# Kernel optimization log

Hardware: AMD Instinct MI355X
Metric: run time of the kernel (lower is better)

Reference implementation:

```python
import math
import jax, jax.numpy as jnp
import numpy as np

DILATIONS = (1, 2, 3)

def conv2d(x, w, b, d=1, p=0):
    # x: NCHW, w: OIHW
    y = jax.lax.conv_general_dilated(
        x, w, window_strides=(1, 1), padding=[(p, p), (p, p)],
        rhs_dilation=(d, d), dimension_numbers=('NCHW', 'OIHW', 'NCHW'))
    return y + b[None, :, None, None]

def setup_inputs() -> dict:
    key = jax.random.key(0)
    ks = jax.random.split(key, 6)
    B, C, H = 2, 256, 96
    inner = 256 // 18  # = 14
    f = lambda k, s, sc: jax.random.normal(k, s, dtype=jnp.float32) * sc
    return {
        'x':        f(ks[0], (B, C, H, H), 1.0),
        'proj_w':   f(ks[1], (C, C, 1, 1), 0.06),
        'proj_b':   jnp.zeros((C,), jnp.float32),
        'reduce_w': f(ks[2], (inner, C, 1, 1), 0.06),
        'reduce_b': jnp.zeros((inner,), jnp.float32),
        'dil_w':    f(ks[3], (3, inner, inner, 3, 3), 0.08),
        'dil_b':    jnp.zeros((3, inner), jnp.float32),
        'fuse_w':   f(ks[4], (C, inner * 3 * 6, 1, 1), 0.06),
        'fuse_b':   jnp.zeros((C,), jnp.float32),
    }

def reference(x, proj_w, proj_b, reduce_w, reduce_b, dil_w, dil_b, fuse_w, fuse_b):
    B, C, H, W = x.shape
    # PatchEmbed (1x1 conv, stride 1) then PatchUnEmbed is identity on layout
    fmap = conv2d(x, proj_w, proj_b)                    # (B,C,H,W)
    # SAMSNLMFilter
    xr = conv2d(fmap, reduce_w, reduce_b)               # (B,inner,H,W)
    tfs = [xr,
           jnp.flip(xr, -1),
           jnp.flip(xr, -2),
           jnp.rot90(xr, 1, (-2, -1)),
           jnp.rot90(xr, 2, (-2, -1)),
           jnp.rot90(xr, 3, (-2, -1))]
    feats = []
    for i, d in enumerate(DILATIONS):
        co = conv2d(xr, dil_w[i], dil_b[i], d=d, p=d)   # (B,inner,H,W)
        feats.extend(co * t for t in tfs)
    fused = conv2d(jnp.concatenate(feats, axis=1), fuse_w, fuse_b)  # (B,C,H,W)
    tok = fused.reshape(B, C, H * W).transpose(0, 2, 1)             # (B,N,C)
    scale = 1.0 / math.sqrt(C)
    scores = jnp.einsum('bnc,bmc->bnm', tok, tok) * scale           # (B,N,N)
    attn = jax.nn.softmax(scores, axis=-1)
    out = jnp.einsum('bnm,bmc->bnc', attn, tok)
    out = out.transpose(0, 2, 1).reshape(B, C, H, W)
    return fmap + 0.2 * out  # residual_scale default 0.2
```

## Files before the change

kernel.cpp:

```cpp
#include <hip/hip_runtime.h>
#include <hip/hip_bf16.h>

#define NB 2
#define CH 256
#define HS 96
#define HW 9216
#define CHW 2359296
#define INNER 14
#define NF 252
#define SL2E 0.09016844f

using f32x4 = __attribute__((ext_vector_type(4))) float;
using s16x8 = __attribute__((ext_vector_type(8))) short;

template<int CIN, typename OT>
__global__ __launch_bounds__(256)
void k_conv1x1(const float* __restrict__ in, const float* __restrict__ w,
               const float* __restrict__ bias, OT* __restrict__ out) {
    __shared__ float wsh[CIN][32];
    const int tid = threadIdx.x;
    const int coB = blockIdx.y * 32;
    for (int e = tid; e < CIN * 32; e += 256) {
        int ci = e >> 5, col = e & 31;
        wsh[ci][col] = w[(coB + col) * CIN + ci];
    }
    __syncthreads();
    const int P0  = blockIdx.x * 512 + tid;
    const int b   = P0 / HW;
    const int pp0 = P0 - b * HW;
    const int pp1 = pp0 + 256;
    const float* inb = in + (size_t)b * CIN * HW;
    float acc0[32], acc1[32];
    #pragma unroll
    for (int j = 0; j < 32; ++j) { acc0[j] = 0.f; acc1[j] = 0.f; }
    for (int ci = 0; ci < CIN; ++ci) {
        float x0 = inb[(size_t)ci * HW + pp0];
        float x1 = inb[(size_t)ci * HW + pp1];
        const float4* wr = (const float4*)wsh[ci];
        #pragma unroll
        for (int q = 0; q < 8; ++q) {
            float4 wv = wr[q];
            acc0[q*4+0] += wv.x*x0; acc0[q*4+1] += wv.y*x0;
            acc0[q*4+2] += wv.z*x0; acc0[q*4+3] += wv.w*x0;
            acc1[q*4+0] += wv.x*x1; acc1[q*4+1] += wv.y*x1;
            acc1[q*4+2] += wv.z*x1; acc1[q*4+3] += wv.w*x1;
        }
    }
    OT* ob = out + (size_t)b * CH * HW;
    #pragma unroll
    for (int j = 0; j < 32; ++j) {
        float bv = bias[coB + j];
        ob[(size_t)(coB + j) * HW + pp0] = (OT)(acc0[j] + bv);
        ob[(size_t)(coB + j) * HW + pp1] = (OT)(acc1[j] + bv);
    }
}

__global__ __launch_bounds__(256)
void k_reduce(const float* __restrict__ fmap, const float* __restrict__ w,
              const float* __restrict__ bias, float* __restrict__ xr) {
    __shared__ float wsh[256][16];
    __shared__ float part[4][64][17];
    const int tid = threadIdx.x;
    for (int e = tid; e < 256 * 16; e += 256) {
        int ci = e >> 4, co = e & 15;
        wsh[ci][co] = (co < INNER) ? w[co * 256 + ci] : 0.f;
    }
    __syncthreads();
    const int px  = tid & 63, grp = tid >> 6;
    const int Pb  = blockIdx.x * 64;
    const int b   = Pb / HW;
    const int ppb = Pb - b * HW;
    const float* fb = fmap + (size_t)b * CHW + (size_t)(grp * 64) * HW + ppb + px;
    float acc[16];
    #pragma unroll
    for (int j = 0; j < 16; ++j) acc[j] = 0.f;
    for (int ci = 0; ci < 64; ++ci) {
        float xv = fb[(size_t)ci * HW];
        const float4* wr = (const float4*)wsh[grp * 64 + ci];
        #pragma unroll
        for (int q = 0; q < 4; ++q) {
            float4 wv = wr[q];
            acc[q*4+0] += wv.x*xv; acc[q*4+1] += wv.y*xv;
            acc[q*4+2] += wv.z*xv; acc[q*4+3] += wv.w*xv;
        }
    }
    #pragma unroll
    for (int j = 0; j < 16; ++j) part[grp][px][j] = acc[j];
    __syncthreads();
    for (int e = tid; e < 64 * INNER; e += 256) {
        int co = e >> 6, p2 = e & 63;
        float v = part[0][p2][co] + part[1][p2][co] + part[2][p2][co] +
                  part[3][p2][co] + bias[co];
        xr[(size_t)(b * INNER + co) * HW + ppb + p2] = v;
    }
}

__global__ __launch_bounds__(256)
void k_dil(const float* __restrict__ xr, const float* __restrict__ dw,
           const float* __restrict__ db, float* __restrict__ feats) {
    int bid = blockIdx.x;
    const int hb = bid % 36; bid /= 36;
    const int oc = bid % 14; bid /= 14;
    const int b  = bid & 1;  bid >>= 1;
    const int d  = bid;
    const int dil = d + 1;
    __shared__ float wsh[126];
    const int tid = threadIdx.x;
    if (tid < 126) wsh[tid] = dw[(d * 14 + oc) * 126 + tid];
    __syncthreads();
    const int p = hb * 256 + tid;
    const int h = p / 96, w = p - (p / 96) * 96;
    const float* xb = xr + (size_t)b * INNER * HW;
    float acc = db[d * 14 + oc];
    for (int ic = 0; ic < 14; ++ic) {
        const float* xc = xb + (size_t)ic * HW;
        #pragma unroll
        for (int kh = 0; kh < 3; ++kh) {
            int ih = h + (kh - 1) * dil;
            if (ih < 0 || ih >= 96) continue;
            #pragma unroll
            for (int kw = 0; kw < 3; ++kw) {
                int iw = w + (kw - 1) * dil;
                if (iw < 0 || iw >= 96) continue;
                acc += xc[ih * 96 + iw] * wsh[ic * 9 + kh * 3 + kw];
            }
        }
    }
    const float* xo = xb + (size_t)oc * HW;
    const int H1 = 95;
    float t0 = xo[h * 96 + w];
    float t1 = xo[h * 96 + (H1 - w)];
    float t2 = xo[(H1 - h) * 96 + w];
    float t3 = xo[w * 96 + (H1 - h)];
    float t4 = xo[(H1 - h) * 96 + (H1 - w)];
    float t5 = xo[(H1 - w) * 96 + h];
    float* fo = feats + (size_t)b * NF * HW;
    const int ch0 = d * 6 * 14 + oc;
    fo[(size_t)(ch0 + 0 * 14) * HW + p] = acc * t0;
    fo[(size_t)(ch0 + 1 * 14) * HW + p] = acc * t1;
    fo[(size_t)(ch0 + 2 * 14) * HW + p] = acc * t2;
    fo[(size_t)(ch0 + 3 * 14) * HW + p] = acc * t3;
    fo[(size_t)(ch0 + 4 * 14) * HW + p] = acc * t4;
    fo[(size_t)(ch0 + 5 * 14) * HW + p] = acc * t5;
}

__global__ __launch_bounds__(256)
void k_tr(const unsigned short* __restrict__ tc, unsigned short* __restrict__ tt) {
    const int tid = threadIdx.x;
    int bid = blockIdx.x;
    const int b = bid / 576;
    const int r = bid - b * 576;
    const int t0 = (r >> 2) * 64;
    const int c0 = (r & 3) * 64;
    __shared__ unsigned int T[64][37];
    const unsigned short* tcb = tc + (size_t)b * CHW;
    unsigned short* ttb = tt + (size_t)b * CHW;
    for (int e = tid; e < 2048; e += 256) {
        int to = e & 63, chp = e >> 6;
        unsigned int v0 = tcb[(size_t)(c0 + 2*chp)     * HW + t0 + to];
        unsigned int v1 = tcb[(size_t)(c0 + 2*chp + 1) * HW + t0 + to];
        T[to][chp] = (v1 << 16) | v0;
    }
    __syncthreads();
    for (int e = tid; e < 2048; e += 256) {
        int to = e >> 5, chp = e & 31;
        ((unsigned int*)(ttb + (size_t)(t0 + to) * CH + c0))[chp] = T[to][chp];
    }
}

#define KTILE 64
#define NSTRIP 2
#define TPS 72

__device__ __forceinline__ unsigned int pk_bf16(float lo, float hi) {
    unsigned int l = __bfloat16_as_ushort(__float2bfloat16(lo));
    unsigned int h = __bfloat16_as_ushort(__float2bfloat16(hi));
    return (h << 16) | l;
}

__global__ __launch_bounds__(256, 2)
void k_attn2(const unsigned short* __restrict__ tok_t,
             const unsigned short* __restrict__ tok_c,
             unsigned short* __restrict__ opart, float* __restrict__ oml) {
    __shared__ unsigned short Kt[64][256];
    __shared__ unsigned short Vt[256][64];
    __shared__ unsigned short Psh[4][16][72];
    const int tid  = threadIdx.x;
    const int wid  = tid >> 6;
    const int lane = tid & 63;
    const int lq   = lane & 15;
    const int lg   = lane >> 4;

    const int blk   = blockIdx.x;
    const int rb    = blk % 288;
    const int strip = blk / 288;
    const int qb    = (rb & 7) * 36 + (rb >> 3);
    const int b     = qb / 144;
    const int q0    = (qb - b * 144) * 64;
    const unsigned short* tt = tok_t + (size_t)b * CHW;
    const unsigned short* tc = tok_c + (size_t)b * CHW;

    s16x8 qf[8];
    {
        const unsigned short* qrow = tt + (size_t)(q0 + wid*16 + lq) * CH + 8*lg;
        #pragma unroll
        for (int ks = 0; ks < 8; ++ks)
            qf[ks] = *(const s16x8*)(qrow + 32*ks);
    }
    float m_r = -1e30f, l_r = 0.f;
    f32x4 oacc[16];
    #pragma unroll
    for (int ct = 0; ct < 16; ++ct) oacc[ct] = (f32x4){0.f,0.f,0.f,0.f};

    s16x8 rk[8], rv[8];
    const int t0k = strip * TPS;
    {
        const int k0 = t0k * KTILE;
        #pragma unroll
        for (int i = 0; i < 8; ++i) {
            int e = i * 256 + tid;
            int key = e >> 5, cho = (e & 31) * 8;
            rk[i] = *(const s16x8*)(tt + (size_t)(k0 + key) * CH + cho);
            int ch = e >> 3, ko = (e & 7) * 8;
            rv[i] = *(const s16x8*)(tc + (size_t)ch * HW + k0 + ko);
        }
    }

    for (int t = 0; t < TPS; ++t) {
        __syncthreads();
        #pragma unroll
        for (int i = 0; i < 8; ++i) {
            int e = i * 256 + tid;
            int key = e >> 5, cho = (e & 31) * 8;
            *(s16x8*)(&Kt[key][cho ^ ((key & 7) << 3)]) = rk[i];
            int ch = e >> 3, ko = (e & 7) * 8;
            *(s16x8*)(&Vt[ch][ko ^ ((ch & 7) << 3)]) = rv[i];
        }
        __syncthreads();
        if (t + 1 < TPS) {
            const int kn = (t0k + t + 1) * KTILE;
            #pragma unroll
            for (int i = 0; i < 8; ++i) {
                int e = i * 256 + tid;
                int key = e >> 5, cho = (e & 31) * 8;
                rk[i] = *(const s16x8*)(tt + (size_t)(kn + key) * CH + cho);
                int ch = e >> 3, ko = (e & 7) * 8;
                rv[i] = *(const s16x8*)(tc + (size_t)ch * HW + kn + ko);
            }
        }
        float s[16];
        #pragma unroll
        for (int mt = 0; mt < 4; ++mt) {
            f32x4 acc = (f32x4){0.f,0.f,0.f,0.f};
            const int key = mt * 16 + lq;
            const int sw  = (key & 7) << 3;
            #pragma unroll
            for (int ks = 0; ks < 8; ++ks) {
                s16x8 af = *(const s16x8*)(&Kt[key][(ks*32 + 8*lg) ^ sw]);
                acc = __builtin_amdgcn_mfma_f32_16x16x32_bf16(af, qf[ks], acc, 0, 0, 0);
            }
            #pragma unroll
            for (int r = 0; r < 4; ++r) s[mt*4 + r] = acc[r] * SL2E;
        }
        float tm = s[0];
        #pragma unroll
        for (int i = 1; i < 16; ++i) tm = fmaxf(tm, s[i]);
        tm = fmaxf(tm, __shfl_xor(tm, 16));
        tm = fmaxf(tm, __shfl_xor(tm, 32));
        const float mn = fmaxf(m_r, tm);
        if (!__all(mn - m_r <= 8.0f)) {
            const float alpha = exp2f(m_r - mn);
            m_r = mn;
            l_r *= alpha;
            #pragma unroll
            for (int ct = 0; ct < 16; ++ct) {
                oacc[ct][0] *= alpha; oacc[ct][1] *= alpha;
                oacc[ct][2] *= alpha; oacc[ct][3] *= alpha;
            }
        }
        float ps = 0.f;
        #pragma unroll
        for (int i = 0; i < 16; ++i) { s[i] = exp2f(s[i] - m_r); ps += s[i]; }
        ps += __shfl_xor(ps, 16);
        ps += __shfl_xor(ps, 32);
        l_r += ps;
        #pragma unroll
        for (int kt = 0; kt < 4; ++kt) {
            *(unsigned int*)&Psh[wid][lq][16*kt + 4*lg]     = pk_bf16(s[kt*4+0], s[kt*4+1]);
            *(unsigned int*)&Psh[wid][lq][16*kt + 4*lg + 2] = pk_bf16(s[kt*4+2], s[kt*4+3]);
        }
        s16x8 pb0 = *(const s16x8*)&Psh[wid][lq][8*lg];
        s16x8 pb1 = *(const s16x8*)&Psh[wid][lq][32 + 8*lg];
        #pragma unroll
        for (int ct = 0; ct < 16; ++ct) {
            const int ch = ct * 16 + lq;
            const int sw = (ch & 7) << 3;
            s16x8 va0 = *(const s16x8*)(&Vt[ch][(8*lg) ^ sw]);
            s16x8 va1 = *(const s16x8*)(&Vt[ch][(32 + 8*lg) ^ sw]);
            oacc[ct] = __builtin_amdgcn_mfma_f32_16x16x32_bf16(va0, pb0, oacc[ct], 0, 0, 0);
            oacc[ct] = __builtin_amdgcn_mfma_f32_16x16x32_bf16(va1, pb1, oacc[ct], 0, 0, 0);
        }
    }
    const float linv = 1.f / l_r;
    const int qi = (strip * 288 + qb) * 64 + wid * 16 + lq;
    unsigned short* op = opart + (size_t)qi * CH;
    #pragma unroll
    for (int ct = 0; ct < 16; ++ct) {
        const int ch0 = ct * 16 + 4 * lg;
        unsigned int* dst = (unsigned int*)(op + ch0);
        dst[0] = pk_bf16(oacc[ct][0] * linv, oacc[ct][1] * linv);
        dst[1] = pk_bf16(oacc[ct][2] * linv, oacc[ct][3] * linv);
    }
    if (lg == 0) {
        oml[(size_t)qi * 2 + 0] = m_r;
        oml[(size_t)qi * 2 + 1] = l_r;
    }
}

__global__ __launch_bounds__(256)
void k_merge(const unsigned short* __restrict__ opart, const float* __restrict__ oml,
             const float* __restrict__ fmap, float* __restrict__ outp) {
    const int qb  = blockIdx.x;
    const int b   = qb / 144;
    const int q0g = (qb - b * 144) * 64;
    const int q   = threadIdx.x & 63;
    const int p   = threadIdx.x >> 6;
    const int qi0 = qb * 64 + q;
    const int qi1 = (288 + qb) * 64 + q;
    const float m0 = oml[(size_t)qi0*2], l0 = oml[(size_t)qi0*2+1];
    const float m1 = oml[(size_t)qi1*2], l1 = oml[(size_t)qi1*2+1];
    const float m  = fmaxf(m0, m1);
    float w0 = exp2f(m0 - m) * l0;
    float w1 = exp2f(m1 - m) * l1;
    const float inv = 1.f / (w0 + w1);
    w0 *= inv; w1 *= inv;
    const unsigned short* o0 = opart + (size_t)qi0 * CH;
    const unsigned short* o1 = opart + (size_t)qi1 * CH;
    const float* fb = fmap + (size_t)b * CHW;
    float* ob = outp + (size_t)b * CHW;
    #pragma unroll 4
    for (int j = 0; j < 16; ++j) {
        const int ch = p * 64 + j * 4;
        ushort4 a = *(const ushort4*)(o0 + ch);
        ushort4 c = *(const ushort4*)(o1 + ch);
        float av[4] = {
            __uint_as_float((unsigned)a.x << 16), __uint_as_float((unsigned)a.y << 16),
            __uint_as_float((unsigned)a.z << 16), __uint_as_float((unsigned)a.w << 16)};
        float cv[4] = {
            __uint_as_float((unsigned)c.x << 16), __uint_as_float((unsigned)c.y << 16),
            __uint_as_float((unsigned)c.z << 16), __uint_as_float((unsigned)c.w << 16)};
        #pragma unroll
        for (int r = 0; r < 4; ++r) {
            const size_t g = (size_t)(ch + r) * HW + q0g + q;
            ob[g] = fb[g] + 0.2f * (w0 * av[r] + w1 * cv[r]);
        }
    }
}

extern "C" void kernel_launch(void* const* d_in, const int* in_sizes, int n_in,
                              void* d_out, int out_size, void* d_ws, size_t ws_size,
                              hipStream_t stream) {
    const float* x        = (const float*)d_in[0];
    const float* proj_w   = (const float*)d_in[1];
    const float* proj_b   = (const float*)d_in[2];
    const float* reduce_w = (const float*)d_in[3];
    const float* reduce_b = (const float*)d_in[4];
    const float* dil_w    = (const float*)d_in[5];
    const float* dil_b    = (const float*)d_in[6];
    const float* fuse_w   = (const float*)d_in[7];
    const float* fuse_b   = (const float*)d_in[8];
    float* out = (float*)d_out;

    float* ws    = (float*)d_ws;
    float* fmap  = ws;
    float* xr    = fmap + 4718592;
    float* feats = xr + 258048;
    unsigned short* tok_c = (unsigned short*)(feats + 4644864);
    unsigned short* tok_t = tok_c + 4718592;
    unsigned short* opart = tok_t + 4718592;
    float* oml = (float*)(opart + 9437184);

    k_conv1x1<256, float><<<dim3(36, 8), 256, 0, stream>>>(x, proj_w, proj_b, fmap);
    k_reduce<<<288, 256, 0, stream>>>(fmap, reduce_w, reduce_b, xr);
    k_dil<<<3024, 256, 0, stream>>>(xr, dil_w, dil_b, feats);
    k_conv1x1<252, __hip_bfloat16><<<dim3(36, 8), 256, 0, stream>>>(
        feats, fuse_w, fuse_b, (__hip_bfloat16*)tok_c);
    k_tr<<<1152, 256, 0, stream>>>(tok_c, tok_t);
    k_attn2<<<576, 256, 0, stream>>>(tok_t, tok_c, opart, oml);
    k_merge<<<288, 256, 0, stream>>>(opart, oml, fmap, out);
}
```

Baseline: 735.8 us.

## Double query rows per attention block and load K/V tiles directly to LDS

Each attention block now covers 128 queries, with each wave handling two 16-row groups, so every K/V tile staged in shared memory is reused twice as much. The grid shrinks from 576 to 288 blocks. The register-staged prefetch of K/V is replaced by global_load_lds direct-to-LDS copies with the XOR swizzle moved into the global address. The accumulator registers double, which may hurt occupancy, and there is no longer any prefetch overlap between tile loads and compute. The lower block count also risks underfilling the GPU's compute units.

```diff
diff --git a/kernel.cpp b/kernel.cpp
--- a/kernel.cpp
+++ b/kernel.cpp
@@ -12,6 +12,13 @@
 
 using f32x4 = __attribute__((ext_vector_type(4))) float;
 using s16x8 = __attribute__((ext_vector_type(8))) short;
+
+__device__ __forceinline__ void gload_lds16(const unsigned short* g, unsigned short* l) {
+    __builtin_amdgcn_global_load_lds(
+        (const __attribute__((address_space(1))) unsigned int*)g,
+        (__attribute__((address_space(3))) unsigned int*)l,
+        16, 0, 0);
+}
 
 template<int CIN, typename OT>
 __global__ __launch_bounds__(256)
@@ -169,7 +176,6 @@
 }
 
 #define KTILE 64
-#define NSTRIP 2
 #define TPS 72
 
 __device__ __forceinline__ unsigned int pk_bf16(float lo, float hi) {
@@ -179,7 +185,7 @@
 }
 
 __global__ __launch_bounds__(256, 2)
-void k_attn2(const unsigned short* __restrict__ tok_t,
+void k_attn3(const unsigned short* __restrict__ tok_t,
              const unsigned short* __restrict__ tok_c,
              unsigned short* __restrict__ opart, float* __restrict__ oml) {
     __shared__ unsigned short Kt[64][256];
@@ -192,128 +198,129 @@
     const int lg   = lane >> 4;
 
     const int blk   = blockIdx.x;
-    const int rb    = blk % 288;
-    const int strip = blk / 288;
-    const int qb    = (rb & 7) * 36 + (rb >> 3);
-    const int b     = qb / 144;
-    const int q0    = (qb - b * 144) * 64;
+    const int strip = blk / 144;
+    const int rb    = blk % 144;
+    const int qb    = (rb & 7) * 18 + (rb >> 3);
+    const int b     = qb / 72;
+    const int n0    = (qb - b * 72) * 128;
     const unsigned short* tt = tok_t + (size_t)b * CHW;
     const unsigned short* tc = tok_c + (size_t)b * CHW;
 
-    s16x8 qf[8];
-    {
-        const unsigned short* qrow = tt + (size_t)(q0 + wid*16 + lq) * CH + 8*lg;
+    s16x8 qf[2][8];
+    #pragma unroll
+    for (int g = 0; g < 2; ++g) {
+        const unsigned short* qrow =
+            tt + (size_t)(n0 + wid*32 + g*16 + lq) * CH + 8*lg;
         #pragma unroll
         for (int ks = 0; ks < 8; ++ks)
-            qf[ks] = *(const s16x8*)(qrow + 32*ks);
-    }
-    float m_r = -1e30f, l_r = 0.f;
-    f32x4 oacc[16];
-    #pragma unroll
-    for (int ct = 0; ct < 16; ++ct) oacc[ct] = (f32x4){0.f,0.f,0.f,0.f};
-
-    s16x8 rk[8], rv[8];
+            qf[g][ks] = *(const s16x8*)(qrow + 32*ks);
+    }
+    float m_r[2] = {-1e30f, -1e30f}, l_r[2] = {0.f, 0.f};
+    f32x4 oacc[2][16];
+    #pragma unroll
+    for (int g = 0; g < 2; ++g)
+        #pragma unroll
+        for (int ct = 0; ct < 16; ++ct) oacc[g][ct] = (f32x4){0.f,0.f,0.f,0.f};
+
+    unsigned short* KtF = &Kt[0][0];
+    unsigned short* VtF = &Vt[0][0];
     const int t0k = strip * TPS;
-    {
-        const int k0 = t0k * KTILE;
+
+    for (int t = 0; t < TPS; ++t) {
+        const int k0 = (t0k + t) * KTILE;
+        __syncthreads();
         #pragma unroll
         for (int i = 0; i < 8; ++i) {
             int e = i * 256 + tid;
             int key = e >> 5, cho = (e & 31) * 8;
-            rk[i] = *(const s16x8*)(tt + (size_t)(k0 + key) * CH + cho);
+            gload_lds16(tt + (size_t)(k0 + key) * CH + (cho ^ ((key & 7) << 3)),
+                        KtF + e * 8);
             int ch = e >> 3, ko = (e & 7) * 8;
-            rv[i] = *(const s16x8*)(tc + (size_t)ch * HW + k0 + ko);
-        }
-    }
-
-    for (int t = 0; t < TPS; ++t) {
+            gload_lds16(tc + (size_t)ch * HW + k0 + (ko ^ ((ch & 7) << 3)),
+                        VtF + e * 8);
+        }
         __syncthreads();
-        #pragma unroll
-        for (int i = 0; i < 8; ++i) {
-            int e = i * 256 + tid;
-            int key = e >> 5, cho = (e & 31) * 8;
-            *(s16x8*)(&Kt[key][cho ^ ((key & 7) << 3)]) = rk[i];
-            int ch = e >> 3, ko = (e & 7) * 8;
-            *(s16x8*)(&Vt[ch][ko ^ ((ch & 7) << 3)]) = rv[i];
-        }
-        __syncthreads();
-        if (t + 1 < TPS) {
-            const int kn = (t0k + t + 1) * KTILE;
-            #pragma unroll
-            for (int i = 0; i < 8; ++i) {
-                int e = i * 256 + tid;
-                int key = e >> 5, cho = (e & 31) * 8;
-                rk[i] = *(const s16x8*)(tt + (size_t)(kn + key) * CH + cho);
-                int ch = e >> 3, ko = (e & 7) * 8;
-                rv[i] = *(const s16x8*)(tc + (size_t)ch * HW + kn + ko);
-            }
-        }
-        float s[16];
+
+        float s[2][16];
         #pragma unroll
         for (int mt = 0; mt < 4; ++mt) {
-            f32x4 acc = (f32x4){0.f,0.f,0.f,0.f};
+            f32x4 a0 = (f32x4){0.f,0.f,0.f,0.f};
+            f32x4 a1 = (f32x4){0.f,0.f,0.f,0.f};
             const int key = mt * 16 + lq;
             const int sw  = (key & 7) << 3;
             #pragma unroll
             for (int ks = 0; ks < 8; ++ks) {
                 s16x8 af = *(const s16x8*)(&Kt[key][(ks*32 + 8*lg) ^ sw]);
-                acc = __builtin_amdgcn_mfma_f32_16x16x32_bf16(af, qf[ks], acc, 0, 0, 0);
-            }
-            #pragma unroll
-            for (int r = 0; r < 4; ++r) s[mt*4 + r] = acc[r] * SL2E;
-        }
-        float tm = s[0];
-        #pragma unroll
-        for (int i = 1; i < 16; ++i) tm = fmaxf(tm, s[i]);
-        tm = fmaxf(tm, __shfl_xor(tm, 16));
-        tm = fmaxf(tm, __shfl_xor(tm, 32));
-        const float mn = fmaxf(m_r, tm);
-        if (!__all(mn - m_r <= 8.0f)) {
-            const float alpha = exp2f(m_r - mn);
-            m_r = mn;
-            l_r *= alpha;
-            #pragma unroll
-            for (int ct = 0; ct < 16; ++ct) {
-                oacc[ct][0] *= alpha; oacc[ct][1] *= alpha;
-                oacc[ct][2] *= alpha; oacc[ct][3] *= alpha;
-            }
-        }
-        float ps = 0.f;
-        #pragma unroll
-        for (int i = 0; i < 16; ++i) { s[i] = exp2f(s[i] - m_r); ps += s[i]; }
-        ps += __shfl_xor(ps, 16);
-        ps += __shfl_xor(ps, 32);
-        l_r += ps;
-        #pragma unroll
-        for (int kt = 0; kt < 4; ++kt) {
-            *(unsigned int*)&Psh[wid][lq][16*kt + 4*lg]     = pk_bf16(s[kt*4+0], s[kt*4+1]);
-            *(unsigned int*)&Psh[wid][lq][16*kt + 4*lg + 2] = pk_bf16(s[kt*4+2], s[kt*4+3]);
-        }
-        s16x8 pb0 = *(const s16x8*)&Psh[wid][lq][8*lg];
-        s16x8 pb1 = *(const s16x8*)&Psh[wid][lq][32 + 8*lg];
+                a0 = __builtin_amdgcn_mfma_f32_16x16x32_bf16(af, qf[0][ks], a0, 0, 0, 0);
+                a1 = __builtin_amdgcn_mfma_f32_16x16x32_bf16(af, qf[1][ks], a1, 0, 0, 0);
+            }
+            #pragma unroll
+            for (int r = 0; r < 4; ++r) {
+                s[0][mt*4 + r] = a0[r] * SL2E;
+                s[1][mt*4 + r] = a1[r] * SL2E;
+            }
+        }
+        s16x8 pb[2][2];
+        #pragma unroll
+        for (int g = 0; g < 2; ++g) {
+            float tm = s[g][0];
+            #pragma unroll
+            for (int i = 1; i < 16; ++i) tm = fmaxf(tm, s[g][i]);
+            tm = fmaxf(tm, __shfl_xor(tm, 16));
+            tm = fmaxf(tm, __shfl_xor(tm, 32));
+            const float mn = fmaxf(m_r[g], tm);
+            if (!__all(mn - m_r[g] <= 8.0f)) {
+                const float alpha = exp2f(m_r[g] - mn);
+                m_r[g] = mn;
+                l_r[g] *= alpha;
+                #pragma unroll
+                for (int ct = 0; ct < 16; ++ct) {
+                    oacc[g][ct][0] *= alpha; oacc[g][ct][1] *= alpha;
+                    oacc[g][ct][2] *= alpha; oacc[g][ct][3] *= alpha;
+                }
+            }
+            float ps = 0.f;
+            #pragma unroll
+            for (int i = 0; i < 16; ++i) { s[g][i] = exp2f(s[g][i] - m_r[g]); ps += s[g][i]; }
+            ps += __shfl_xor(ps, 16);
+            ps += __shfl_xor(ps, 32);
+            l_r[g] += ps;
+            #pragma unroll
+            for (int kt = 0; kt < 4; ++kt) {
+                *(unsigned int*)&Psh[wid][lq][16*kt + 4*lg]     = pk_bf16(s[g][kt*4+0], s[g][kt*4+1]);
+                *(unsigned int*)&Psh[wid][lq][16*kt + 4*lg + 2] = pk_bf16(s[g][kt*4+2], s[g][kt*4+3]);
+            }
+            pb[g][0] = *(const s16x8*)&Psh[wid][lq][8*lg];
+            pb[g][1] = *(const s16x8*)&Psh[wid][lq][32 + 8*lg];
+        }
         #pragma unroll
         for (int ct = 0; ct < 16; ++ct) {
             const int ch = ct * 16 + lq;
             const int sw = (ch & 7) << 3;
             s16x8 va0 = *(const s16x8*)(&Vt[ch][(8*lg) ^ sw]);
             s16x8 va1 = *(const s16x8*)(&Vt[ch][(32 + 8*lg) ^ sw]);
-            oacc[ct] = __builtin_amdgcn_mfma_f32_16x16x32_bf16(va0, pb0, oacc[ct], 0, 0, 0);
-            oacc[ct] = __builtin_amdgcn_mfma_f32_16x16x32_bf16(va1, pb1, oacc[ct], 0, 0, 0);
-        }
-    }
-    const float linv = 1.f / l_r;
-    const int qi = (strip * 288 + qb) * 64 + wid * 16 + lq;
-    unsigned short* op = opart + (size_t)qi * CH;
-    #pragma unroll
-    for (int ct = 0; ct < 16; ++ct) {
-        const int ch0 = ct * 16 + 4 * lg;
-        unsigned int* dst = (unsigned int*)(op + ch0);
-        dst[0] = pk_bf16(oacc[ct][0] * linv, oacc[ct][1] * linv);
-        dst[1] = pk_bf16(oacc[ct][2] * linv, oacc[ct][3] * linv);
-    }
-    if (lg == 0) {
-        oml[(size_t)qi * 2 + 0] = m_r;
-        oml[(size_t)qi * 2 + 1] = l_r;
+            oacc[0][ct] = __builtin_amdgcn_mfma_f32_16x16x32_bf16(va0, pb[0][0], oacc[0][ct], 0, 0, 0);
+            oacc[0][ct] = __builtin_amdgcn_mfma_f32_16x16x32_bf16(va1, pb[0][1], oacc[0][ct], 0, 0, 0);
+            oacc[1][ct] = __builtin_amdgcn_mfma_f32_16x16x32_bf16(va0, pb[1][0], oacc[1][ct], 0, 0, 0);
+            oacc[1][ct] = __builtin_amdgcn_mfma_f32_16x16x32_bf16(va1, pb[1][1], oacc[1][ct], 0, 0, 0);
+        }
+    }
+    #pragma unroll
+    for (int g = 0; g < 2; ++g) {
+        const float linv = 1.f / l_r[g];
+        const int qi = strip * (NB * HW) + b * HW + n0 + wid*32 + g*16 + lq;
+        unsigned short* op = opart + (size_t)qi * CH;
+        #pragma unroll
+        for (int ct = 0; ct < 16; ++ct) {
+            const int ch0 = ct * 16 + 4 * lg;
+            unsigned int* dst = (unsigned int*)(op + ch0);
+            dst[0] = pk_bf16(oacc[g][ct][0] * linv, oacc[g][ct][1] * linv);
+            dst[1] = pk_bf16(oacc[g][ct][2] * linv, oacc[g][ct][3] * linv);
+        }
+        if (lg == 0) {
+            oml[(size_t)qi * 2 + 0] = m_r[g];
+            oml[(size_t)qi * 2 + 1] = l_r[g];
+        }
     }
 }
 
@@ -326,7 +333,7 @@
     const int q   = threadIdx.x & 63;
     const int p   = threadIdx.x >> 6;
     const int qi0 = qb * 64 + q;
-    const int qi1 = (288 + qb) * 64 + q;
+    const int qi1 = NB * HW + qi0;
     const float m0 = oml[(size_t)qi0*2], l0 = oml[(size_t)qi0*2+1];
     const float m1 = oml[(size_t)qi1*2], l1 = oml[(size_t)qi1*2+1];
     const float m  = fmaxf(m0, m1);
@@ -386,6 +393,6 @@
     k_conv1x1<252, __hip_bfloat16><<<dim3(36, 8), 256, 0, stream>>>(
         feats, fuse_w, fuse_b, (__hip_bfloat16*)tok_c);
     k_tr<<<1152, 256, 0, stream>>>(tok_c, tok_t);
-    k_attn2<<<576, 256, 0, stream>>>(tok_t, tok_c, opart, oml);
+    k_attn3<<<288, 256, 0, stream>>>(tok_t, tok_c, opart, oml);
     k_merge<<<288, 256, 0, stream>>>(opart, oml, fmap, out);
 }
```

Result: slower. 852.5 us (+15.9%).
